# Performance work log

Measured on AMD Instinct MI355X. Metric: run time of the kernel, lower is better.

The kernel has to match this reference:

```python
import jax, jax.numpy as jnp
import numpy as np

B_BOX, N_CLASS = 2, 20          # B, C from __init__
LAMBDA_C, LAMBDA_N = 5.0, 0.5   # self.lambda_c, self.lambda_n
GRID = 49                        # hard-coded 7x7 grid


def setup_inputs() -> dict:
    key = jax.random.key(0)
    k1, k2 = jax.random.split(key)
    outputs = jax.random.uniform(k1, (16384, GRID, 5 * B_BOX + N_CLASS), dtype=jnp.float32)
    target = jax.random.uniform(k2, (16384, 10, 5), dtype=jnp.float32)
    return {"outputs": outputs, "target": target}


def _forward(outputs, target):
    batch, n_obj = target.shape[0], target.shape[1]
    Bb = B_BOX
    # --- target preprocessing: sqrt(w,h), nan -> -1 ---
    tgt = target.at[:, :, 2:4].set(jnp.sqrt(target[:, :, 2:4]))
    tgt = jnp.nan_to_num(tgt, nan=-1.0)
    # --- grid-cell assignment (vectorized version of the batch*obj python loop) ---
    x, y = tgt[:, :, 0], tgt[:, :, 1]
    xi = jnp.trunc(7.0 * x).astype(jnp.int32)   # int(7*x) truncation semantics
    yi = jnp.trunc(7.0 * y).astype(jnp.int32)
    cell = jnp.clip(7 * yi + xi, 0, GRID - 1)
    valid = ((x != -1.0) & (xi >= 0)).astype(tgt.dtype)
    sel = jax.nn.one_hot(cell, GRID, dtype=tgt.dtype) * valid[..., None]   # [b,obj,49]
    ti = sel[:, :, :, None] * tgt[:, :, None, :]                           # [b,obj,49,5]
    ti = jnp.transpose(ti, (0, 2, 1, 3))                                   # [b,49,obj,5]
    # --- permute: move first Bb nonzero boxes of each cell to the top ---
    nonzero = jnp.sum(ti, axis=-1) > 0                                     # [b,49,obj]
    slot = jnp.cumsum(nonzero.astype(jnp.int32), axis=-1) - 1
    slot = jnp.where(nonzero, jnp.minimum(slot, Bb), Bb)                   # Bb = discard slot
    oh = jax.nn.one_hot(slot, Bb + 1, dtype=ti.dtype)                      # [b,49,obj,Bb+1]
    gt = jnp.einsum('bcos,bcod->bcsd', oh, ti)[:, :, :Bb]                  # [b,49,Bb,5]
    # --- iou_matrix (boxes stored as center +/- (sqrt_wh)^2 corners) ---
    pred5 = outputs[:, :, :5 * Bb].reshape(batch, GRID, Bb, 5)
    pdims = pred5[..., :4]
    pdims = pdims.at[..., 2:4].set(jnp.sqrt(pdims[..., 2:4]))
    gdims = gt[..., :4]
    gmin, gmax = gdims[..., :2] - gdims[..., 2:4] ** 2, gdims[..., :2] + gdims[..., 2:4] ** 2
    pmin, pmax = pdims[..., :2] - pdims[..., 2:4] ** 2, pdims[..., :2] + pdims[..., 2:4] ** 2
    # pairwise: axis2 = pred box, axis3 = gt box
    imin = jnp.maximum(gmin[:, :, None, :, :], pmin[:, :, :, None, :])
    imax = jnp.minimum(gmax[:, :, None, :, :], pmax[:, :, :, None, :])
    d = jnp.maximum(imax - imin, 0.0)
    inter = d[..., 0] * d[..., 1]                                          # [b,49,Bb,Bb]
    gwh, pwh = jnp.abs(gmax - gmin), jnp.abs(pmax - pmin)
    garea = (gwh[..., 0] * gwh[..., 1])[:, :, None, :]
    parea = (pwh[..., 0] * pwh[..., 1])[:, :, :, None]
    union = garea + parea - inter
    iou = jnp.where(union == 0, 0.0, inter / jnp.where(union == 0, 1.0, union))  # nan_to_num(i/u)
    t_index = jnp.argmax(iou, axis=2)                                      # [b,49,Bb]
    # --- construct_model_ground_truth: gather assigned gt box + truncated-int confidence ---
    idx = jnp.broadcast_to(t_index[..., None], gt.shape)
    gathered = jnp.take_along_axis(gt, idx, axis=2)                        # [b,49,Bb,5]
    r1wh, r2wh = pred5[..., 2:4] ** 2, gathered[..., 2:4] ** 2
    min1, max1 = pred5[..., :2] - 0.5 * r1wh, pred5[..., :2] + 0.5 * r1wh
    min2, max2 = gathered[..., :2] - 0.5 * r2wh, gathered[..., :2] + 0.5 * r2wh
    d2 = jnp.maximum(jnp.minimum(max1, max2) - jnp.maximum(min1, min2), 0.0)
    inter2 = d2[..., 0] * d2[..., 1]
    union2 = r1wh[..., 0] * r1wh[..., 1] + r2wh[..., 0] * r2wh[..., 1] - inter2
    conf = jnp.where((jnp.trunc(union2) == 0) | (jnp.trunc(inter2) == 0), 0.0,
                     jnp.trunc(inter2 / jnp.where(union2 == 0, 1.0, union2)))
    final_gt = gathered.at[..., 4].set(conf)
    # --- obj loss: lambda_c on x,y,w,h; 1.0 on confidence ---
    w = jnp.array([LAMBDA_C, LAMBDA_C, LAMBDA_C, LAMBDA_C, 1.0], dtype=outputs.dtype)
    obj_loss = jnp.sum(w * (final_gt - pred5) ** 2)
    # --- noobj loss (faithfully replicates original bug: mask is recreated per loop
    #     iteration, so only the last (batch, bbox) iteration's mask survives) ---
    pconf, gconf = pred5[..., 4], final_gt[..., 4]                         # [b,49,Bb]
    mask = jnp.ones_like(gconf)
    mask = mask.at[batch - 1, jnp.arange(GRID), t_index[batch - 1, :, Bb - 1]].set(0.0)
    noobj_loss = LAMBDA_N * jnp.sum(((pconf - gconf) * mask) ** 2)
    # --- class loss ---
    cls_scores = outputs[:, :, 5 * Bb:]                                    # [b,49,C]
    max_pred = jnp.max(cls_scores, axis=2)[..., None]                      # [b,49,1]
    pred_cls = jnp.argmax(cls_scores, axis=2)[..., None]                   # [b,49,1]
    predictions = max_pred * pconf                                         # [b,49,Bb]
    truths = (final_gt[..., 4] == pred_cls.astype(outputs.dtype)).astype(outputs.dtype)
    cell_mask = jnp.sign(jnp.sum(final_gt, axis=-1))                       # [b,49,Bb]
    class_loss = jnp.sum(cell_mask * (truths - predictions) ** 2)
    return (obj_loss + noobj_loss + class_loss) / batch


def reference(outputs, target):
    return _forward(outputs, target)
```

## Files before the change

### kernel.cpp

```cpp
#include <hip/hip_runtime.h>
#include <math.h>

#define GRID_CELLS 49
#define NOBJ 10
#define BB 2
#define NCLS 20
#define OUT_C 30
#define LAMBDA_C 5.0f
#define LAMBDA_N 0.5f
#define BLOCK 256
#define WAVES (BLOCK / 64)
#define CELLW 10
#define ROWW (GRID_CELLS * OUT_C)

__global__ __launch_bounds__(BLOCK) void yolo_loss_wave(
    const float* __restrict__ outputs,
    const float* __restrict__ target,
    float* __restrict__ out,
    int batch, float inv_batch)
{
    __shared__ __align__(16) float rows[WAVES][ROWW];
    __shared__ float gt[WAVES][GRID_CELLS][CELLW];
    __shared__ float red[WAVES];

    const int t = threadIdx.x;
    const int w = t >> 6;
    const int lane = t & 63;
    const int b = blockIdx.x * WAVES + w;

    float lsum = 0.0f;
    if (b < batch) {
        {
            const float2* src = reinterpret_cast<const float2*>(outputs + (size_t)b * ROWW);
            float2* dst = reinterpret_cast<float2*>(&rows[w][0]);
            #pragma unroll
            for (int i = 0; i < 12; ++i) {
                int idx = i * 64 + lane;
                if (idx < ROWW / 2) dst[idx] = src[idx];
            }
        }
        {
            float* gz = &gt[w][0][0];
            #pragma unroll
            for (int i = 0; i < 8; ++i) {
                int idx = i * 64 + lane;
                if (idx < GRID_CELLS * CELLW) gz[idx] = 0.0f;
            }
        }
        float t0 = 0.f, t1 = 0.f, t2f = 0.f, t3f = 0.f, t4 = 0.f;
        int cell = 0, nz = 0;
        if (lane < NOBJ) {
            const float* tp = target + (size_t)b * (NOBJ * 5) + lane * 5;
            t0 = tp[0]; t1 = tp[1];
            t2f = sqrtf(tp[2]); t3f = sqrtf(tp[3]);
            t4 = tp[4];
            if (t0 != t0)   t0  = -1.0f;
            if (t1 != t1)   t1  = -1.0f;
            if (t2f != t2f) t2f = -1.0f;
            if (t3f != t3f) t3f = -1.0f;
            if (t4 != t4)   t4  = -1.0f;
            int xi = (int)truncf(7.0f * t0);
            int yi = (int)truncf(7.0f * t1);
            cell = 7 * yi + xi;
            cell = cell < 0 ? 0 : (cell > GRID_CELLS - 1 ? GRID_CELLS - 1 : cell);
            bool valid = (t0 != -1.0f) && (xi >= 0);
            float s5 = t0 + t1 + t2f + t3f + t4;
            nz = (valid && (s5 > 0.0f)) ? 1 : 0;
        }
        int slot = 0;
        #pragma unroll
        for (int p = 0; p < NOBJ - 1; ++p) {
            int cp = __shfl(cell, p, 64);
            int np = __shfl(nz, p, 64);
            if (p < lane && np && cp == cell) slot++;
        }
        if (lane < NOBJ && nz && slot < BB) {
            gt[w][cell][slot * 5 + 0] = t0;
            gt[w][cell][slot * 5 + 1] = t1;
            gt[w][cell][slot * 5 + 2] = t2f;
            gt[w][cell][slot * 5 + 3] = t3f;
            gt[w][cell][slot * 5 + 4] = t4;
        }
        asm volatile("s_waitcnt lgkmcnt(0)" ::: "memory");

        if (lane < GRID_CELLS) {
            const int c = lane;
            float g[BB][5];
            #pragma unroll
            for (int s = 0; s < BB; ++s)
                #pragma unroll
                for (int d = 0; d < 5; ++d) g[s][d] = gt[w][c][s * 5 + d];

            const float2* r2 = reinterpret_cast<const float2*>(&rows[w][c * OUT_C]);
            float pred[BB][5];
            {
                float2 p0 = r2[0], p1 = r2[1], p2 = r2[2], p3 = r2[3], p4 = r2[4];
                pred[0][0] = p0.x; pred[0][1] = p0.y; pred[0][2] = p1.x; pred[0][3] = p1.y; pred[0][4] = p2.x;
                pred[1][0] = p2.y; pred[1][1] = p3.x; pred[1][2] = p3.y; pred[1][3] = p4.x; pred[1][4] = p4.y;
            }
            float maxp; int cls;
            {
                float2 q0 = r2[5];
                maxp = q0.x; cls = 0;
                if (q0.y > maxp) { maxp = q0.y; cls = 1; }
                #pragma unroll
                for (int i = 1; i < NCLS / 2; ++i) {
                    float2 q = r2[5 + i];
                    if (q.x > maxp) { maxp = q.x; cls = 2 * i; }
                    if (q.y > maxp) { maxp = q.y; cls = 2 * i + 1; }
                }
            }
            float fcls = (float)cls;

            float pminx[BB], pmaxx[BB], pminy[BB], pmaxy[BB], parea[BB];
            #pragma unroll
            for (int p = 0; p < BB; ++p) {
                float sw = sqrtf(pred[p][2]);
                float sh = sqrtf(pred[p][3]);
                float w2 = sw * sw, h2 = sh * sh;
                pminx[p] = pred[p][0] - w2; pmaxx[p] = pred[p][0] + w2;
                pminy[p] = pred[p][1] - h2; pmaxy[p] = pred[p][1] + h2;
                parea[p] = fabsf(pmaxx[p] - pminx[p]) * fabsf(pmaxy[p] - pminy[p]);
            }
            float gminx[BB], gmaxx[BB], gminy[BB], gmaxy[BB], garea[BB];
            #pragma unroll
            for (int s = 0; s < BB; ++s) {
                float w2 = g[s][2] * g[s][2], h2 = g[s][3] * g[s][3];
                gminx[s] = g[s][0] - w2; gmaxx[s] = g[s][0] + w2;
                gminy[s] = g[s][1] - h2; gmaxy[s] = g[s][1] + h2;
                garea[s] = fabsf(gmaxx[s] - gminx[s]) * fabsf(gmaxy[s] - gminy[s]);
            }
            int t_index[BB];
            #pragma unroll
            for (int s = 0; s < BB; ++s) {
                float best = 0.0f; int bi = 0;
                #pragma unroll
                for (int p = 0; p < BB; ++p) {
                    float ix0 = fmaxf(gminx[s], pminx[p]);
                    float iy0 = fmaxf(gminy[s], pminy[p]);
                    float ix1 = fminf(gmaxx[s], pmaxx[p]);
                    float iy1 = fminf(gmaxy[s], pmaxy[p]);
                    float dx = fmaxf(ix1 - ix0, 0.0f);
                    float dy = fmaxf(iy1 - iy0, 0.0f);
                    float inter = dx * dy;
                    float uni = garea[s] + parea[p] - inter;
                    float iou = (uni == 0.0f) ? 0.0f : inter / uni;
                    if (p == 0) { best = iou; bi = 0; }
                    else if (iou > best) { best = iou; bi = p; }
                }
                t_index[s] = bi;
            }

            #pragma unroll
            for (int s = 0; s < BB; ++s) {
                float ga[5];
                #pragma unroll
                for (int d = 0; d < 5; ++d) ga[d] = (t_index[s] == 0) ? g[0][d] : g[1][d];
                float r1w = pred[s][2] * pred[s][2], r1h = pred[s][3] * pred[s][3];
                float r2w = ga[2] * ga[2],           r2h = ga[3] * ga[3];
                float min1x = pred[s][0] - 0.5f * r1w, max1x = pred[s][0] + 0.5f * r1w;
                float min1y = pred[s][1] - 0.5f * r1h, max1y = pred[s][1] + 0.5f * r1h;
                float min2x = ga[0] - 0.5f * r2w, max2x = ga[0] + 0.5f * r2w;
                float min2y = ga[1] - 0.5f * r2h, max2y = ga[1] + 0.5f * r2h;
                float dx = fmaxf(fminf(max1x, max2x) - fmaxf(min1x, min2x), 0.0f);
                float dy = fmaxf(fminf(max1y, max2y) - fmaxf(min1y, min2y), 0.0f);
                float inter2 = dx * dy;
                float uni2 = r1w * r1h + r2w * r2h - inter2;
                float conf;
                if (truncf(uni2) == 0.0f || truncf(inter2) == 0.0f) conf = 0.0f;
                else conf = truncf(inter2 / (uni2 == 0.0f ? 1.0f : uni2));
                #pragma unroll
                for (int d = 0; d < 4; ++d) {
                    float df = ga[d] - pred[s][d];
                    lsum += LAMBDA_C * df * df;
                }
                { float df = conf - pred[s][4]; lsum += df * df; }
                float m = 1.0f;
                if (b == batch - 1 && s == t_index[BB - 1]) m = 0.0f;
                float dn = (pred[s][4] - conf) * m;
                lsum += LAMBDA_N * dn * dn;
                float predn = maxp * pred[s][4];
                float truth = (conf == fcls) ? 1.0f : 0.0f;
                float sum5 = ga[0] + ga[1] + ga[2] + ga[3] + conf;
                float cm = (sum5 > 0.0f) ? 1.0f : ((sum5 < 0.0f) ? -1.0f : 0.0f);
                float dcl = truth - predn;
                lsum += cm * dcl * dcl;
            }
        }
    }

    #pragma unroll
    for (int off = 32; off > 0; off >>= 1) lsum += __shfl_down(lsum, off, 64);
    if (lane == 0) red[w] = lsum;
    __syncthreads();
    if (t == 0) {
        float s = 0.0f;
        #pragma unroll
        for (int v = 0; v < WAVES; ++v) s += red[v];
        atomicAdd(out, s * inv_batch);
    }
}

extern "C" void kernel_launch(void* const* d_in, const int* in_sizes, int n_in,
                              void* d_out, int out_size, void* d_ws, size_t ws_size,
                              hipStream_t stream) {
    const float* outputs = (const float*)d_in[0];
    const float* target  = (const float*)d_in[1];
    float* out = (float*)d_out;
    int batch = in_sizes[1] / (NOBJ * 5);
    int nblocks = (batch + WAVES - 1) / WAVES;
    hipMemsetAsync(out, 0, sizeof(float), stream);
    yolo_loss_wave<<<nblocks, BLOCK, 0, stream>>>(outputs, target, out, batch, 1.0f / (float)batch);
}
```

Baseline: 175.1 us.

## Map one thread per grid cell across five images with persistent grid-stride blocks

Replaces the one-wave-per-image layout, which staged each output row through shared memory and left 15 of 64 lanes idle, with a mapping of 245 threads to five images times 49 cells. Each thread loads its 30 floats straight into registers. Target preprocessing for all five images runs in wave 0, and occupancy bitmasks replace zero-filling the shared gt array. A capped grid of 2048 blocks loops over image groups, so fewer atomics are issued, at the cost of two block barriers per group and strided, uncoalesced per-thread global loads.

```diff
diff --git a/kernel.cpp b/kernel.cpp
--- a/kernel.cpp
+++ b/kernel.cpp
@@ -9,103 +9,125 @@
 #define LAMBDA_C 5.0f
 #define LAMBDA_N 0.5f
 #define BLOCK 256
-#define WAVES (BLOCK / 64)
+#define ITEMS 5
 #define CELLW 10
-#define ROWW (GRID_CELLS * OUT_C)
-
-__global__ __launch_bounds__(BLOCK) void yolo_loss_wave(
+
+__global__ __launch_bounds__(BLOCK, 4) void yolo_loss_v9(
     const float* __restrict__ outputs,
     const float* __restrict__ target,
     float* __restrict__ out,
-    int batch, float inv_batch)
+    int batch, float inv_batch, int ngroups)
 {
-    __shared__ __align__(16) float rows[WAVES][ROWW];
-    __shared__ float gt[WAVES][GRID_CELLS][CELLW];
-    __shared__ float red[WAVES];
+    __shared__ float gt[ITEMS][GRID_CELLS][CELLW];
+    __shared__ unsigned int msk[ITEMS][4];
+    __shared__ float red[BLOCK / 64];
 
     const int t = threadIdx.x;
-    const int w = t >> 6;
+    const int wv = t >> 6;
     const int lane = t & 63;
-    const int b = blockIdx.x * WAVES + w;
-
-    float lsum = 0.0f;
-    if (b < batch) {
-        {
-            const float2* src = reinterpret_cast<const float2*>(outputs + (size_t)b * ROWW);
-            float2* dst = reinterpret_cast<float2*>(&rows[w][0]);
-            #pragma unroll
-            for (int i = 0; i < 12; ++i) {
-                int idx = i * 64 + lane;
-                if (idx < ROWW / 2) dst[idx] = src[idx];
-            }
+
+    float acc = 0.0f;
+
+    for (int grp = blockIdx.x; grp < ngroups; grp += gridDim.x) {
+        const int b0 = grp * ITEMS;
+        const int li = t / GRID_CELLS;
+        const int c  = t - li * GRID_CELLS;
+        const int b  = b0 + li;
+        const bool isLoss = (t < ITEMS * GRID_CELLS) && (b < batch);
+
+        float2 rv[15];
+        if (isLoss) {
+            const float2* r2 = reinterpret_cast<const float2*>(
+                outputs + (size_t)(b * GRID_CELLS + c) * OUT_C);
+            #pragma unroll
+            for (int i = 0; i < 15; ++i) rv[i] = r2[i];
         }
-        {
-            float* gz = &gt[w][0][0];
-            #pragma unroll
-            for (int i = 0; i < 8; ++i) {
-                int idx = i * 64 + lane;
-                if (idx < GRID_CELLS * CELLW) gz[idx] = 0.0f;
+
+        if (wv == 0) {
+            const int o   = lane % NOBJ;
+            const int pli = lane / NOBJ;
+            const int pb  = b0 + pli;
+            float t0 = 0.f, t1 = 0.f, t2f = 0.f, t3f = 0.f, t4 = 0.f;
+            int cell = 0, nz = 0;
+            if (lane < ITEMS * NOBJ && pb < batch) {
+                const float* tp = target + (size_t)pb * (NOBJ * 5) + o * 5;
+                t0 = tp[0]; t1 = tp[1];
+                t2f = sqrtf(tp[2]); t3f = sqrtf(tp[3]);
+                t4 = tp[4];
+                if (t0 != t0)   t0  = -1.0f;
+                if (t1 != t1)   t1  = -1.0f;
+                if (t2f != t2f) t2f = -1.0f;
+                if (t3f != t3f) t3f = -1.0f;
+                if (t4 != t4)   t4  = -1.0f;
+                int xi = (int)truncf(7.0f * t0);
+                int yi = (int)truncf(7.0f * t1);
+                cell = 7 * yi + xi;
+                cell = cell < 0 ? 0 : (cell > GRID_CELLS - 1 ? GRID_CELLS - 1 : cell);
+                bool valid = (t0 != -1.0f) && (xi >= 0);
+                float s5 = t0 + t1 + t2f + t3f + t4;
+                nz = (valid && (s5 > 0.0f)) ? 1 : 0;
+            }
+            int packed = cell | (nz << 8);
+            int slot = 0;
+            #pragma unroll
+            for (int p = 0; p < NOBJ - 1; ++p) {
+                int pk = __shfl(packed, lane - o + p, 64);
+                if (p < o && (pk >> 8) && (pk & 0xff) == cell) slot++;
+            }
+            unsigned int m0lo = 0, m0hi = 0, m1lo = 0, m1hi = 0;
+            if (nz) {
+                if (cell < 32) m0lo = 1u << cell; else m0hi = 1u << (cell - 32);
+                if (slot == 1) {
+                    if (cell < 32) m1lo = 1u << cell; else m1hi = 1u << (cell - 32);
+                }
+            }
+            #pragma unroll
+            for (int off = 1; off < 16; off <<= 1) {
+                unsigned int a = __shfl(m0lo, lane + off, 64);
+                unsigned int bq = __shfl(m0hi, lane + off, 64);
+                unsigned int cq = __shfl(m1lo, lane + off, 64);
+                unsigned int dq = __shfl(m1hi, lane + off, 64);
+                if (o + off < NOBJ) { m0lo |= a; m0hi |= bq; m1lo |= cq; m1hi |= dq; }
+            }
+            if (lane < ITEMS * NOBJ && pb < batch && o == 0) {
+                msk[pli][0] = m0lo; msk[pli][1] = m0hi;
+                msk[pli][2] = m1lo; msk[pli][3] = m1hi;
+            }
+            if (lane < ITEMS * NOBJ && pb < batch && nz && slot < BB) {
+                gt[pli][cell][slot * 5 + 0] = t0;
+                gt[pli][cell][slot * 5 + 1] = t1;
+                gt[pli][cell][slot * 5 + 2] = t2f;
+                gt[pli][cell][slot * 5 + 3] = t3f;
+                gt[pli][cell][slot * 5 + 4] = t4;
             }
         }
-        float t0 = 0.f, t1 = 0.f, t2f = 0.f, t3f = 0.f, t4 = 0.f;
-        int cell = 0, nz = 0;
-        if (lane < NOBJ) {
-            const float* tp = target + (size_t)b * (NOBJ * 5) + lane * 5;
-            t0 = tp[0]; t1 = tp[1];
-            t2f = sqrtf(tp[2]); t3f = sqrtf(tp[3]);
-            t4 = tp[4];
-            if (t0 != t0)   t0  = -1.0f;
-            if (t1 != t1)   t1  = -1.0f;
-            if (t2f != t2f) t2f = -1.0f;
-            if (t3f != t3f) t3f = -1.0f;
-            if (t4 != t4)   t4  = -1.0f;
-            int xi = (int)truncf(7.0f * t0);
-            int yi = (int)truncf(7.0f * t1);
-            cell = 7 * yi + xi;
-            cell = cell < 0 ? 0 : (cell > GRID_CELLS - 1 ? GRID_CELLS - 1 : cell);
-            bool valid = (t0 != -1.0f) && (xi >= 0);
-            float s5 = t0 + t1 + t2f + t3f + t4;
-            nz = (valid && (s5 > 0.0f)) ? 1 : 0;
-        }
-        int slot = 0;
-        #pragma unroll
-        for (int p = 0; p < NOBJ - 1; ++p) {
-            int cp = __shfl(cell, p, 64);
-            int np = __shfl(nz, p, 64);
-            if (p < lane && np && cp == cell) slot++;
-        }
-        if (lane < NOBJ && nz && slot < BB) {
-            gt[w][cell][slot * 5 + 0] = t0;
-            gt[w][cell][slot * 5 + 1] = t1;
-            gt[w][cell][slot * 5 + 2] = t2f;
-            gt[w][cell][slot * 5 + 3] = t3f;
-            gt[w][cell][slot * 5 + 4] = t4;
-        }
-        asm volatile("s_waitcnt lgkmcnt(0)" ::: "memory");
-
-        if (lane < GRID_CELLS) {
-            const int c = lane;
+        __syncthreads();
+
+        if (isLoss) {
+            const unsigned int m0lo = msk[li][0], m0hi = msk[li][1];
+            const unsigned int m1lo = msk[li][2], m1hi = msk[li][3];
+            const bool has0 = (c < 32) ? ((m0lo >> c) & 1u) : ((m0hi >> (c - 32)) & 1u);
+            const bool has1 = (c < 32) ? ((m1lo >> c) & 1u) : ((m1hi >> (c - 32)) & 1u);
             float g[BB][5];
             #pragma unroll
-            for (int s = 0; s < BB; ++s)
-                #pragma unroll
-                for (int d = 0; d < 5; ++d) g[s][d] = gt[w][c][s * 5 + d];
-
-            const float2* r2 = reinterpret_cast<const float2*>(&rows[w][c * OUT_C]);
+            for (int d = 0; d < 5; ++d) g[0][d] = has0 ? gt[li][c][d] : 0.0f;
+            #pragma unroll
+            for (int d = 0; d < 5; ++d) g[1][d] = has1 ? gt[li][c][5 + d] : 0.0f;
+
             float pred[BB][5];
             {
-                float2 p0 = r2[0], p1 = r2[1], p2 = r2[2], p3 = r2[3], p4 = r2[4];
+                float2 p0 = rv[0], p1 = rv[1], p2 = rv[2], p3 = rv[3], p4 = rv[4];
                 pred[0][0] = p0.x; pred[0][1] = p0.y; pred[0][2] = p1.x; pred[0][3] = p1.y; pred[0][4] = p2.x;
                 pred[1][0] = p2.y; pred[1][1] = p3.x; pred[1][2] = p3.y; pred[1][3] = p4.x; pred[1][4] = p4.y;
             }
             float maxp; int cls;
             {
-                float2 q0 = r2[5];
+                float2 q0 = rv[5];
                 maxp = q0.x; cls = 0;
                 if (q0.y > maxp) { maxp = q0.y; cls = 1; }
                 #pragma unroll
                 for (int i = 1; i < NCLS / 2; ++i) {
-                    float2 q = r2[5 + i];
+                    float2 q = rv[5 + i];
                     if (q.x > maxp) { maxp = q.x; cls = 2 * i; }
                     if (q.y > maxp) { maxp = q.y; cls = 2 * i + 1; }
                 }
@@ -151,6 +173,7 @@
                 t_index[s] = bi;
             }
 
+            float lsum = 0.0f;
             #pragma unroll
             for (int s = 0; s < BB; ++s) {
                 float ga[5];
@@ -186,17 +209,19 @@
                 float dcl = truth - predn;
                 lsum += cm * dcl * dcl;
             }
+            acc += lsum;
         }
+        __syncthreads();
     }
 
     #pragma unroll
-    for (int off = 32; off > 0; off >>= 1) lsum += __shfl_down(lsum, off, 64);
-    if (lane == 0) red[w] = lsum;
+    for (int off = 32; off > 0; off >>= 1) acc += __shfl_down(acc, off, 64);
+    if (lane == 0) red[wv] = acc;
     __syncthreads();
     if (t == 0) {
         float s = 0.0f;
         #pragma unroll
-        for (int v = 0; v < WAVES; ++v) s += red[v];
+        for (int v = 0; v < BLOCK / 64; ++v) s += red[v];
         atomicAdd(out, s * inv_batch);
     }
 }
@@ -208,7 +233,9 @@
     const float* target  = (const float*)d_in[1];
     float* out = (float*)d_out;
     int batch = in_sizes[1] / (NOBJ * 5);
-    int nblocks = (batch + WAVES - 1) / WAVES;
+    int ngroups = (batch + ITEMS - 1) / ITEMS;
+    int nblocks = ngroups < 2048 ? ngroups : 2048;
     hipMemsetAsync(out, 0, sizeof(float), stream);
-    yolo_loss_wave<<<nblocks, BLOCK, 0, stream>>>(outputs, target, out, batch, 1.0f / (float)batch);
+    yolo_loss_v9<<<nblocks, BLOCK, 0, stream>>>(outputs, target, out, batch,
+                                                1.0f / (float)batch, ngroups);
 }
```

New measurement: 151.3 us. 13.6% less time.
